# Kernel optimization log

Measured on AMD Instinct MI355X. Metric: run time of the kernel, lower is better.

Reference implementation:

```python
import jax, jax.numpy as jnp
import numpy as np

B, S, H, NH, HD, ROT = 4, 1024, 2048, 16, 128, 64
P = NH * HD  # attention projection size = 2048
EPS = 1e-6


def setup_inputs() -> dict:
    key = jax.random.key(0)
    ks = jax.random.split(key, 12)
    T = B * S
    # rotary frequency table [max_pos=S, 1, ROT]
    inv_freq = 1.0 / (10000.0 ** (np.arange(0, ROT, 2, dtype=np.float32) / ROT))
    f = np.outer(np.arange(S, dtype=np.float32), inv_freq)  # [S, ROT/2]
    freqs = np.concatenate([f, f], axis=-1)[:, None, :].astype(np.float32)
    sc = 0.02
    return {
        "positions": jnp.tile(jnp.arange(S, dtype=jnp.int64), B),  # per-seq positions 0..S-1
        "hidden_states": jax.random.normal(ks[0], (T, H), jnp.float32),
        "rotary_pos_emb": jnp.asarray(freqs),
        "lf1_cache": jax.random.normal(ks[1], (B, 1, H), jnp.float32) * sc,
        "lf2_cache": jax.random.normal(ks[2], (B, 1, H // 2), jnp.float32) * sc,
        "Wqk": jax.random.normal(ks[3], (2 * P, H), jnp.float32) * sc,
        "Wv": jax.random.normal(ks[4], (P, H), jnp.float32) * sc,
        "Wo": jax.random.normal(ks[5], (H, P), jnp.float32) * sc,
        "conv1_w": jax.random.normal(ks[6], (H // 2, H, 2), jnp.float32) * sc,  # [out, in, tap]
        "conv1_b": jnp.zeros((H // 2,), jnp.float32),
        "conv2_w": jax.random.normal(ks[7], (H, H // 2, 2), jnp.float32) * sc,
        "conv2_b": jnp.zeros((H,), jnp.float32),
        "ln_g": jnp.ones((H,), jnp.float32),
    }


def reference(positions, hidden_states, rotary_pos_emb, lf1_cache, lf2_cache,
              Wqk, Wv, Wo, conv1_w, conv1_b, conv2_w, conv2_b, ln_g):
    T = hidden_states.shape[0]
    scaling = HD ** -0.5

    # v projection on raw hidden states (done before lf_gate in the source)
    v = hidden_states @ Wv.T  # [T, P]

    # ---- LocalizedFiltering (two causal 2-tap convs + residual + RMSNorm),
    # vectorized over all sequences (source loops per sequence) ----
    x = hidden_states.reshape(B, S, H)
    xc = jnp.concatenate([lf1_cache, x], axis=1)  # [B, S+1, H]
    o1 = (jnp.einsum('bsh,oh->bso', xc[:, :-1], conv1_w[..., 0])
          + jnp.einsum('bsh,oh->bso', xc[:, 1:], conv1_w[..., 1]) + conv1_b)  # [B,S,H/2]
    o1c = jnp.concatenate([lf2_cache, o1], axis=1)  # [B, S+1, H/2]
    o2 = (jnp.einsum('bsc,oc->bso', o1c[:, :-1], conv2_w[..., 0])
          + jnp.einsum('bsc,oc->bso', o1c[:, 1:], conv2_w[..., 1]) + conv2_b)  # [B,S,H]
    o3 = o2 + x
    lf = o3 * jax.lax.rsqrt(jnp.mean(o3 * o3, axis=-1, keepdims=True) + EPS) * ln_g

    hs = lf.reshape(T, H)
    qk = (hs @ Wqk.T).reshape(T, NH, 2 * HD)
    q, k = jnp.split(qk, 2, axis=-1)  # each [T, NH, HD]

    # partial rotary (mscale = 1.0 since use_yarn=False)
    f = rotary_pos_emb[positions]            # [T, 1, ROT]
    cos, sin = jnp.cos(f), jnp.sin(f)

    def rope(t):
        tr, tp = t[..., :ROT], t[..., ROT:]
        t1, t2 = jnp.split(tr, 2, axis=-1)
        rot = jnp.concatenate([-t2, t1], axis=-1)
        return jnp.concatenate([tr * cos + rot * sin, tp], axis=-1)

    qb = rope(q).reshape(B, S, NH, HD)
    kb = rope(k).reshape(B, S, NH, HD)
    vb = v.reshape(B, S, NH, HD)

    # causal attention per sequence
    scores = jnp.einsum('bqhd,bkhd->bhqk', qb, kb) * scaling
    mask = jnp.tril(jnp.ones((S, S), bool))
    scores = jnp.where(mask, scores, jnp.finfo(scores.dtype).min)
    attn = jax.nn.softmax(scores, axis=-1)
    out = jnp.einsum('bhqk,bkhd->bqhd', attn, vb).reshape(T, P)
    return out @ Wo.T  # [T, H]
```

## Files before the change

### kernel.cpp

```cpp
#include <hip/hip_runtime.h>

typedef __bf16 bf16;
typedef __bf16 bf16x8 __attribute__((ext_vector_type(8)));
typedef __bf16 bf16x4 __attribute__((ext_vector_type(4)));
typedef float f32x4 __attribute__((ext_vector_type(4)));

#define DEVI __device__ __forceinline__

constexpr int Bc = 4, Sc = 1024, Hc = 2048, NHc = 16, HDc = 128;
constexpr int Tc = Bc * Sc;
constexpr int Pc = NHc * HDc;

DEVI void async16(const void* g, void* l) {
  __builtin_amdgcn_global_load_lds(
      (const __attribute__((address_space(1))) unsigned int*)g,
      (__attribute__((address_space(3))) unsigned int*)l, 16, 0, 0);
}

template <int WM, int WN, int MREP, int NREP, bool OUT_BF16>
__global__ __launch_bounds__(WM * WN * 64, 2) void gemm_pipe(
    const bf16* __restrict__ A, const bf16* __restrict__ W, void* __restrict__ Cout,
    const float* __restrict__ bias, int M, int N, int K) {
  constexpr int BM = WM * MREP * 16;
  constexpr int BN = WN * NREP * 16;
  constexpr int THREADS = WM * WN * 64;
  constexpr int ROWS = BM + BN;
  constexpr int CHA = BM * 4 / THREADS;
  constexpr int CHB = BN * 4 / THREADS;
  static_assert(CHA + CHB == 4, "vmcnt ledger assumes 4 loads/thread/stage");
  __shared__ bf16 lds[4][ROWS * 32];

  const int nbx = N / BN;
  const int nwg = (M / BM) * nbx;
  const int wgid = (blockIdx.x & 7) * (nwg >> 3) + (blockIdx.x >> 3);
  const int bx = wgid % nbx, by = wgid / nbx;
  const int m0 = by * BM, n0 = bx * BN;
  const int tid = threadIdx.x;
  const int w = tid >> 6, l = tid & 63;
  const int wm = w / WN, wn = w % WN;
  const int lr = l & 15;
  const int hi = l >> 4;

  auto stage = [&](int slot, int t) {
    const int k0 = t << 5;
#pragma unroll
    for (int c = 0; c < CHA; ++c) {
      const int ch = c * THREADS + tid;
      const int row = ch >> 2, cg = ch & 3;
      const int gc = (cg ^ ((row >> 1) & 3)) << 3;
      async16(A + (size_t)(m0 + row) * K + k0 + gc, (char*)&lds[slot][0] + ch * 16);
    }
#pragma unroll
    for (int c = 0; c < CHB; ++c) {
      const int ch = c * THREADS + tid;
      const int row = ch >> 2, cg = ch & 3;
      const int gc = (cg ^ ((row >> 1) & 3)) << 3;
      async16(W + (size_t)(n0 + row) * K + k0 + gc,
              (char*)&lds[slot][0] + (BM * 4 + ch) * 16);
    }
  };

  f32x4 acc[MREP][NREP] = {};
  const int nk = K >> 5;

  stage(0, 0);
  stage(1, 1);
  stage(2, 2);
  asm volatile("s_waitcnt vmcnt(8)" ::: "memory");
  __builtin_amdgcn_s_barrier();
  __builtin_amdgcn_sched_barrier(0);

  bf16x8 fAc[MREP], fBc[NREP], fAn[MREP], fBn[NREP];
  {
    const char* nb = (const char*)&lds[0][0];
#pragma unroll
    for (int mi = 0; mi < MREP; ++mi) {
      const int r = wm * (MREP * 16) + mi * 16 + lr;
      fAc[mi] = *(const bf16x8*)(nb + r * 64 + ((hi ^ ((r >> 1) & 3)) << 4));
    }
#pragma unroll
    for (int ni = 0; ni < NREP; ++ni) {
      const int r = BM + wn * (NREP * 16) + ni * 16 + lr;
      fBc[ni] = *(const bf16x8*)(nb + r * 64 + ((hi ^ ((r >> 1) & 3)) << 4));
    }
  }

#define GSTEP(T_, CA, CB, NA, NB)                                              \
  do {                                                                         \
    if ((T_) + 2 < nk) asm volatile("s_waitcnt vmcnt(4)" ::: "memory");        \
    else               asm volatile("s_waitcnt vmcnt(0)" ::: "memory");        \
    __builtin_amdgcn_s_barrier();                                              \
    __builtin_amdgcn_sched_barrier(0);                                         \
    if ((T_) + 3 < nk) stage(((T_) + 3) & 3, (T_) + 3);                        \
    if ((T_) + 1 < nk) {                                                       \
      const char* nb = (const char*)&lds[((T_) + 1) & 3][0];                   \
      _Pragma("unroll") for (int mi = 0; mi < MREP; ++mi) {                    \
        const int r = wm * (MREP * 16) + mi * 16 + lr;                         \
        NA[mi] = *(const bf16x8*)(nb + r * 64 + ((hi ^ ((r >> 1) & 3)) << 4)); \
      }                                                                        \
      _Pragma("unroll") for (int ni = 0; ni < NREP; ++ni) {                    \
        const int r = BM + wn * (NREP * 16) + ni * 16 + lr;                    \
        NB[ni] = *(const bf16x8*)(nb + r * 64 + ((hi ^ ((r >> 1) & 3)) << 4)); \
      }                                                                        \
    }                                                                          \
    __builtin_amdgcn_s_setprio(1);                                             \
    _Pragma("unroll") for (int mi = 0; mi < MREP; ++mi)                        \
      _Pragma("unroll") for (int ni = 0; ni < NREP; ++ni)                      \
        acc[mi][ni] =                                                          \
            __builtin_amdgcn_mfma_f32_16x16x32_bf16(CA[mi], CB[ni], acc[mi][ni], 0, 0, 0); \
    __builtin_amdgcn_s_setprio(0);                                             \
  } while (0)

  for (int t = 0; t < nk; t += 2) {
    GSTEP(t, fAc, fBc, fAn, fBn);
    GSTEP(t + 1, fAn, fBn, fAc, fBc);
  }
#undef GSTEP

#pragma unroll
  for (int ni = 0; ni < NREP; ++ni) {
    const int col = n0 + wn * (NREP * 16) + ni * 16 + lr;
    const float bv = bias ? bias[col] : 0.f;
#pragma unroll
    for (int mi = 0; mi < MREP; ++mi) {
#pragma unroll
      for (int j = 0; j < 4; ++j) {
        const int row = m0 + wm * (MREP * 16) + mi * 16 + (hi << 2) + j;
        const float vv = acc[mi][ni][j] + bv;
        if (OUT_BF16)
          ((bf16*)Cout)[(size_t)row * N + col] = (bf16)vv;
        else
          ((float*)Cout)[(size_t)row * N + col] = vv;
      }
    }
  }
}

__global__ void k_f2b4(const float* __restrict__ in, bf16* __restrict__ out, int n4) {
  int i = blockIdx.x * 256 + threadIdx.x;
  if (i >= n4) return;
  float4 v = ((const float4*)in)[i];
  bf16x4 o = {(bf16)v.x, (bf16)v.y, (bf16)v.z, (bf16)v.w};
  ((bf16x4*)out)[i] = o;
}

__global__ void k_build_a1(const float* __restrict__ hid, const float* __restrict__ lf1,
                           bf16* __restrict__ hsb, bf16* __restrict__ A1) {
  int idx = blockIdx.x * 256 + threadIdx.x;
  int t = idx >> 11, h = idx & 2047;
  float x = hid[idx];
  hsb[idx] = (bf16)x;
  float xp;
  if ((t & (Sc - 1)) == 0)
    xp = lf1[(t >> 10) * Hc + h];
  else
    xp = hid[idx - Hc];
  size_t a = ((size_t)t << 12) + 2 * h;
  A1[a] = (bf16)xp;
  A1[a + 1] = (bf16)x;
}

__global__ void k_build_a2(const bf16* __restrict__ o1, const float* __restrict__ lf2,
                           bf16* __restrict__ A2) {
  int idx = blockIdx.x * 256 + threadIdx.x;
  int t = idx >> 10, c = idx & 1023;
  bf16 cur = o1[idx];
  bf16 prev;
  if ((t & (Sc - 1)) == 0)
    prev = (bf16)lf2[(t >> 10) * 1024 + c];
  else
    prev = o1[idx - 1024];
  size_t a = ((size_t)t << 11) + 2 * c;
  A2[a] = prev;
  A2[a + 1] = cur;
}

__global__ __launch_bounds__(256) void k_rmsnorm(const bf16* __restrict__ o2,
                                                 const float* __restrict__ hid,
                                                 const float* __restrict__ g,
                                                 bf16* __restrict__ lf) {
  int t = blockIdx.x, tid = threadIdx.x;
  size_t base = ((size_t)t << 11) + tid * 8;
  bf16x8 ov = *(const bf16x8*)&o2[base];
  const float* hp = &hid[base];
  float vals[8];
  float ss = 0.f;
#pragma unroll
  for (int i = 0; i < 8; ++i) {
    float x = (float)ov[i] + hp[i];
    vals[i] = x;
    ss += x * x;
  }
#pragma unroll
  for (int off = 1; off < 64; off <<= 1) ss += __shfl_xor(ss, off);
  __shared__ float red[4];
  if ((tid & 63) == 0) red[tid >> 6] = ss;
  __syncthreads();
  float tot = red[0] + red[1] + red[2] + red[3];
  float inv = rsqrtf(tot * (1.f / 2048.f) + 1e-6f);
  bf16x8 o;
#pragma unroll
  for (int i = 0; i < 8; ++i) o[i] = (bf16)(vals[i] * inv * g[tid * 8 + i]);
  *(bf16x8*)&lf[base] = o;
}

__global__ void k_rope(const bf16* __restrict__ qk, const float* __restrict__ rot,
                       bf16* __restrict__ qr, bf16* __restrict__ kr) {
  int bid = blockIdx.x;
  int n = bid & 15, t = bid >> 4;
  int s = t & (Sc - 1), b = t >> 10;
  int tid = threadIdx.x;
  int isk = tid >> 7, d = tid & 127;
  const bf16* src = qk + ((size_t)t << 12) + n * 256 + isk * 128;
  float val = (float)src[d];
  float outv = val;
  if (d < 64) {
    float f = rot[s * 64 + d];
    float c = cosf(f), sn = sinf(f);
    float other = (float)src[d ^ 32];
    outv = (d < 32) ? (val * c - other * sn) : (val * c + other * sn);
  }
  bf16* dst = isk ? kr : qr;
  dst[((size_t)((b * 16 + n) * 1024 + s) << 7) + d] = (bf16)outv;
}

__global__ void k_vt(const bf16* __restrict__ v, bf16* __restrict__ vT) {
  __shared__ bf16 tile[32][33];
  int bid = blockIdx.x;
  int dt = bid & 3;
  int st = (bid >> 2) & 31;
  int bn = bid >> 7;
  int b = bn >> 4, n = bn & 15;
  int tx = threadIdx.x & 31, ty = threadIdx.x >> 5;
#pragma unroll
  for (int i = 0; i < 4; ++i) {
    int s = st * 32 + ty + i * 8;
    int d = dt * 32 + tx;
    tile[ty + i * 8][tx] = v[(size_t)(b * 1024 + s) * 2048 + n * 128 + d];
  }
  __syncthreads();
#pragma unroll
  for (int i = 0; i < 4; ++i) {
    int d = dt * 32 + ty + i * 8;
    int s = st * 32 + tx;
    vT[((size_t)(bn * 128 + d)) * 1024 + s] = tile[tx][ty + i * 8];
  }
}

__global__ __launch_bounds__(256, 2) void k_attn(const bf16* __restrict__ qr,
                                                 const bf16* __restrict__ kr,
                                                 const bf16* __restrict__ vT,
                                                 bf16* __restrict__ att) {
  __shared__ bf16 Ks[2][64 * 128];
  __shared__ bf16 Vs[2][128 * 64];
  __shared__ bf16 plds[4][16 * 64];
  const int bid = blockIdx.x;
  const int xcd = bid & 7, jj = bid >> 3;
  const int bn = xcd * 8 + (jj >> 3);
  const int pr = jj & 7;
  const int tid = threadIdx.x, w = tid >> 6, l = tid & 63;
  const int lr = l & 15, hi = l >> 4;
  const bf16* kb = kr + ((size_t)bn << 17);
  const bf16* vb = vT + ((size_t)bn << 17);
  const int b = bn >> 4, hh = bn & 15;
  const float scaling = 0.08838834764831845f;

  auto stage = [&](int buf, int kt) {
#pragma unroll
    for (int c = 0; c < 4; ++c) {
      int chunk = c * 256 + tid;
      int prow = chunk >> 4, pcg = chunk & 15;
      async16(kb + ((size_t)(kt * 64 + prow) << 7) + ((pcg ^ (prow & 7)) << 3),
              (char*)&Ks[buf][0] + chunk * 16);
    }
#pragma unroll
    for (int c = 0; c < 4; ++c) {
      int chunk = c * 256 + tid;
      int prow = chunk >> 3, pcg = chunk & 7;
      async16(vb + ((size_t)prow << 10) + kt * 64 + ((pcg ^ (prow & 7)) << 3),
              (char*)&Vs[buf][0] + chunk * 16);
    }
  };

#pragma unroll 1
  for (int phase = 0; phase < 2; ++phase) {
    const int qt = phase ? (15 - pr) : pr;
    const int qg0 = qt * 64 + w * 16;
    const bf16* qb = qr + ((size_t)(bn * 1024 + qg0) << 7);
    bf16x8 qf[4];
#pragma unroll
    for (int ks = 0; ks < 4; ++ks) qf[ks] = *(const bf16x8*)&qb[lr * 128 + ks * 32 + hi * 8];
    f32x4 oacc[8] = {};
    float mrow[4] = {-1e30f, -1e30f, -1e30f, -1e30f};
    float lrow[4] = {0.f, 0.f, 0.f, 0.f};
    const int nkb = qt + 1;

    stage(0, 0);
    __syncthreads();

    for (int kbt = 0; kbt < nkb; ++kbt) {
      const int cur = kbt & 1;
      if (kbt + 1 < nkb) stage(cur ^ 1, kbt + 1);

      f32x4 sacc[4] = {};
#pragma unroll
      for (int n = 0; n < 4; ++n) {
        const int krow = n * 16 + lr;
#pragma unroll
        for (int ks = 0; ks < 4; ++ks) {
          bf16x8 kf = *(const bf16x8*)&Ks[cur][(krow << 7) + ((((ks << 2) | hi) ^ (krow & 7)) << 3)];
          sacc[n] = __builtin_amdgcn_mfma_f32_16x16x32_bf16(qf[ks], kf, sacc[n], 0, 0, 0);
        }
      }
      const bool needmask = (kbt * 64 + 63 > qg0);
#pragma unroll
      for (int n = 0; n < 4; ++n) {
        int kg = kbt * 64 + n * 16 + lr;
#pragma unroll
        for (int j = 0; j < 4; ++j) {
          float sv = sacc[n][j] * scaling;
          if (needmask && kg > qg0 + hi * 4 + j) sv = -1e30f;
          sacc[n][j] = sv;
        }
      }
      float sf[4];
#pragma unroll
      for (int j = 0; j < 4; ++j) {
        float pm = fmaxf(fmaxf(sacc[0][j], sacc[1][j]), fmaxf(sacc[2][j], sacc[3][j]));
        pm = fmaxf(pm, __shfl_xor(pm, 1));
        pm = fmaxf(pm, __shfl_xor(pm, 2));
        pm = fmaxf(pm, __shfl_xor(pm, 4));
        pm = fmaxf(pm, __shfl_xor(pm, 8));
        float mn = fmaxf(mrow[j], pm);
        sf[j] = __expf(mrow[j] - mn);
        mrow[j] = mn;
      }
#pragma unroll
      for (int n = 0; n < 4; ++n)
#pragma unroll
        for (int j = 0; j < 4; ++j) sacc[n][j] = __expf(sacc[n][j] - mrow[j]);
#pragma unroll
      for (int j = 0; j < 4; ++j) {
        float ps = sacc[0][j] + sacc[1][j] + sacc[2][j] + sacc[3][j];
        ps += __shfl_xor(ps, 1);
        ps += __shfl_xor(ps, 2);
        ps += __shfl_xor(ps, 4);
        ps += __shfl_xor(ps, 8);
        lrow[j] = lrow[j] * sf[j] + ps;
      }
#pragma unroll
      for (int dt = 0; dt < 8; ++dt)
#pragma unroll
        for (int j = 0; j < 4; ++j) oacc[dt][j] *= sf[j];
#pragma unroll
      for (int n = 0; n < 4; ++n)
#pragma unroll
        for (int j = 0; j < 4; ++j)
          plds[w][(hi * 4 + j) * 64 + n * 16 + lr] = (bf16)sacc[n][j];
      asm volatile("s_waitcnt lgkmcnt(0)" ::: "memory");
#pragma unroll
      for (int ks2 = 0; ks2 < 2; ++ks2) {
        bf16x8 pf = *(const bf16x8*)&plds[w][lr * 64 + ks2 * 32 + hi * 8];
#pragma unroll
        for (int dt = 0; dt < 8; ++dt) {
          const int vrow = dt * 16 + lr;
          bf16x8 vf = *(const bf16x8*)&Vs[cur][(vrow << 6) + ((((ks2 << 2) | hi) ^ (lr & 7)) << 3)];
          oacc[dt] = __builtin_amdgcn_mfma_f32_16x16x32_bf16(pf, vf, oacc[dt], 0, 0, 0);
        }
      }
      __syncthreads();
    }

#pragma unroll
    for (int j = 0; j < 4; ++j) {
      float inv = 1.f / lrow[j];
      int qg = qg0 + hi * 4 + j;
      size_t obase = ((size_t)(b * 1024 + qg) << 11) + hh * 128;
#pragma unroll
      for (int dt = 0; dt < 8; ++dt) att[obase + dt * 16 + lr] = (bf16)(oacc[dt][j] * inv);
    }
  }
}

extern "C" void kernel_launch(void* const* d_in, const int* in_sizes, int n_in,
                              void* d_out, int out_size, void* d_ws, size_t ws_size,
                              hipStream_t stream) {
  const float* hid = (const float*)d_in[1];
  const float* rot = (const float*)d_in[2];
  const float* lf1 = (const float*)d_in[3];
  const float* lf2 = (const float*)d_in[4];
  const float* Wqk = (const float*)d_in[5];
  const float* Wv  = (const float*)d_in[6];
  const float* Wo  = (const float*)d_in[7];
  const float* c1w = (const float*)d_in[8];
  const float* c1b = (const float*)d_in[9];
  const float* c2w = (const float*)d_in[10];
  const float* c2b = (const float*)d_in[11];
  const float* lng = (const float*)d_in[12];
  float* outp = (float*)d_out;
  char* ws = (char*)d_ws;

  const size_t MB = 1ull << 20;
  bf16* Wslot = (bf16*)(ws + 0 * MB);
  bf16* A1    = (bf16*)(ws + 16 * MB);
  bf16* qkb   = A1;
  bf16* hsb   = (bf16*)(ws + 48 * MB);
  bf16* lfb   = hsb;
  bf16* vT    = hsb;
  bf16* v     = (bf16*)(ws + 64 * MB);
  bf16* att   = v;
  bf16* o1    = (bf16*)(ws + 80 * MB);
  bf16* A2    = (bf16*)(ws + 88 * MB);
  bf16* qr    = A2;
  bf16* o2    = (bf16*)(ws + 104 * MB);
  bf16* kr    = o2;

  auto f2b = [&](const float* in, bf16* out, int n) {
    int n4 = n / 4;
    k_f2b4<<<(n4 + 255) / 256, 256, 0, stream>>>(in, out, n4);
  };

  f2b(Wv, Wslot, 2048 * 2048);
  k_build_a1<<<Tc * Hc / 256, 256, 0, stream>>>(hid, lf1, hsb, A1);
  gemm_pipe<2, 2, 4, 4, true><<<512, 256, 0, stream>>>(hsb, Wslot, v, nullptr, Tc, Pc, Hc);

  f2b(c1w, Wslot, 1024 * 2048 * 2);
  gemm_pipe<2, 2, 4, 4, true><<<256, 256, 0, stream>>>(A1, Wslot, o1, c1b, Tc, 1024, 4096);

  k_build_a2<<<Tc * 1024 / 256, 256, 0, stream>>>(o1, lf2, A2);
  f2b(c2w, Wslot, 2048 * 1024 * 2);
  gemm_pipe<2, 2, 4, 4, true><<<512, 256, 0, stream>>>(A2, Wslot, o2, c2b, Tc, 2048, 2048);

  k_rmsnorm<<<Tc, 256, 0, stream>>>(o2, hid, lng, lfb);

  f2b(Wqk, Wslot, 4096 * 2048);
  gemm_pipe<2, 4, 8, 4, true><<<256, 512, 0, stream>>>(lfb, Wslot, qkb, nullptr, Tc, 4096, Hc);

  k_rope<<<Tc * NHc, 256, 0, stream>>>(qkb, rot, qr, kr);
  k_vt<<<64 * 32 * 4, 256, 0, stream>>>(v, vT);
  k_attn<<<Bc * NHc * 8, 256, 0, stream>>>(qr, kr, vT, att);

  f2b(Wo, Wslot, 2048 * 2048);
  gemm_pipe<2, 2, 4, 4, false><<<512, 256, 0, stream>>>(att, Wslot, outp, nullptr, Tc, 2048, 2048);
}
```

Before: 401.9 us.

## Add 8-wave double-buffered GEMM with quadrant-interleaved loads and MFMA

Introduces a new GEMM kernel using 512 threads (8 waves), 256x128 or 256x256 tiles, a 64-wide K step with XOR-swizzled LDS and double buffering. Each K step is split into four quadrant phases that interleave LDS fragment loads, half-tile prefetch of the next stage, and MFMA bursts raised to higher priority. The v, conv2, qk and output projections switch to it with larger tiles and fewer workgroups. The goal is better latency hiding and more data reuse per tile. In exchange the kernel needs more barriers, and a fixed 256-workgroup grid may limit occupancy.

```diff
diff --git a/kernel.cpp b/kernel.cpp
--- a/kernel.cpp
+++ b/kernel.cpp
@@ -15,6 +15,155 @@
   __builtin_amdgcn_global_load_lds(
       (const __attribute__((address_space(1))) unsigned int*)g,
       (__attribute__((address_space(3))) unsigned int*)l, 16, 0, 0);
+}
+
+#define BAR() __builtin_amdgcn_s_barrier()
+#define LGKM0()                                          \
+  do {                                                   \
+    asm volatile("s_waitcnt lgkmcnt(0)" ::: "memory");   \
+    __builtin_amdgcn_sched_barrier(0);                   \
+  } while (0)
+#define VM0() asm volatile("s_waitcnt vmcnt(0)" ::: "memory")
+
+template <int WM, int WN, int MREP, int NREP, bool OUT_BF16>
+__global__ __launch_bounds__(512, 2) void gemm8(
+    const bf16* __restrict__ A, const bf16* __restrict__ W, void* __restrict__ Cout,
+    const float* __restrict__ bias, int M, int N, int K) {
+  constexpr int BM = WM * MREP * 16;
+  constexpr int BN = WN * NREP * 16;
+  constexpr int MH = MREP / 2, NH = NREP / 2;
+  constexpr int LA = BM / 128;
+  constexpr int LB = BN / 128;
+  __shared__ char lds[2][(BM + BN) * 128];
+
+  const int nbx = N / BN;
+  const int nwg = (M / BM) * nbx;
+  const int wgid = (blockIdx.x & 7) * (nwg >> 3) + (blockIdx.x >> 3);
+  const int bx = wgid % nbx, by = wgid / nbx;
+  const int m0 = by * BM, n0 = bx * BN;
+  const int tid = threadIdx.x;
+  const int w = tid >> 6, l = tid & 63;
+  const int wm = w / WN, wn = w % WN;
+  const int lr = l & 15, hi = l >> 4;
+
+  auto stageA = [&](int buf, int t, int half) {
+#pragma unroll
+    for (int c = 0; c < LA; ++c) {
+      const int ch = c * 512 + tid;
+      const int row = half * (BM / 2) + (ch >> 3);
+      const int grp = ch & 7;
+      async16(A + (size_t)(m0 + row) * K + (t << 6) + ((grp ^ (row & 7)) << 3),
+              &lds[buf][row * 128 + grp * 16]);
+    }
+  };
+  auto stageB = [&](int buf, int t, int half) {
+#pragma unroll
+    for (int c = 0; c < LB; ++c) {
+      const int ch = c * 512 + tid;
+      const int row = half * (BN / 2) + (ch >> 3);
+      const int grp = ch & 7;
+      async16(W + (size_t)(n0 + row) * K + (t << 6) + ((grp ^ (row & 7)) << 3),
+              &lds[buf][BM * 128 + row * 128 + grp * 16]);
+    }
+  };
+  auto LD = [&](const char* Lp, int row, int g) -> bf16x8 {
+    return *(const bf16x8*)(Lp + ((size_t)row << 7) + ((g ^ (row & 7)) << 4));
+  };
+
+#define QUAD(MB_, NB_, FB_)                                                     \
+  do {                                                                          \
+    __builtin_amdgcn_s_setprio(1);                                              \
+    _Pragma("unroll") for (int m = 0; m < MH; ++m)                              \
+      _Pragma("unroll") for (int n = 0; n < NH; ++n)                            \
+        _Pragma("unroll") for (int kk = 0; kk < 2; ++kk)                        \
+          acc[(MB_) + m][(NB_) + n] = __builtin_amdgcn_mfma_f32_16x16x32_bf16(  \
+              fa[m][kk], FB_[n][kk], acc[(MB_) + m][(NB_) + n], 0, 0, 0);       \
+    __builtin_amdgcn_s_setprio(0);                                              \
+  } while (0)
+
+  f32x4 acc[MREP][NREP] = {};
+  bf16x8 fa[MH][2], fb0[NH][2], fb1[NH][2];
+  const int nk = K >> 6;
+
+  stageA(0, 0, 0);
+  stageB(0, 0, 0);
+  stageB(0, 0, 1);
+  stageA(0, 0, 1);
+  VM0();
+  BAR();
+
+#pragma unroll 1
+  for (int t = 0; t < nk; ++t) {
+    const char* Lb = lds[t & 1];
+    const int nbuf = (t & 1) ^ 1;
+    const bool pf = (t + 1 < nk);
+#pragma unroll
+    for (int m = 0; m < MH; ++m) {
+      const int r = wm * (MREP * 16) + m * 16 + lr;
+      fa[m][0] = LD(Lb, r, hi);
+      fa[m][1] = LD(Lb, r, 4 + hi);
+    }
+#pragma unroll
+    for (int n = 0; n < NH; ++n) {
+      const int r = BM + wn * (NREP * 16) + n * 16 + lr;
+      fb0[n][0] = LD(Lb, r, hi);
+      fb0[n][1] = LD(Lb, r, 4 + hi);
+    }
+    if (pf) {
+      stageA(nbuf, t + 1, 0);
+      stageB(nbuf, t + 1, 0);
+    }
+    BAR();
+    LGKM0();
+    QUAD(0, 0, fb0);
+    BAR();
+#pragma unroll
+    for (int n = 0; n < NH; ++n) {
+      const int r = BM + wn * (NREP * 16) + (NH + n) * 16 + lr;
+      fb1[n][0] = LD(Lb, r, hi);
+      fb1[n][1] = LD(Lb, r, 4 + hi);
+    }
+    if (pf) {
+      stageB(nbuf, t + 1, 1);
+      stageA(nbuf, t + 1, 1);
+    }
+    BAR();
+    LGKM0();
+    QUAD(0, NH, fb1);
+    BAR();
+#pragma unroll
+    for (int m = 0; m < MH; ++m) {
+      const int r = wm * (MREP * 16) + (MH + m) * 16 + lr;
+      fa[m][0] = LD(Lb, r, hi);
+      fa[m][1] = LD(Lb, r, 4 + hi);
+    }
+    BAR();
+    LGKM0();
+    QUAD(MH, NH, fb1);
+    BAR();
+    QUAD(MH, 0, fb0);
+    VM0();
+    BAR();
+  }
+#undef QUAD
+
+#pragma unroll
+  for (int ni = 0; ni < NREP; ++ni) {
+    const int col = n0 + wn * (NREP * 16) + ni * 16 + lr;
+    const float bv = bias ? bias[col] : 0.f;
+#pragma unroll
+    for (int mi = 0; mi < MREP; ++mi) {
+#pragma unroll
+      for (int j = 0; j < 4; ++j) {
+        const int row = m0 + wm * (MREP * 16) + mi * 16 + (hi << 2) + j;
+        const float vv = acc[mi][ni][j] + bv;
+        if (OUT_BF16)
+          ((bf16*)Cout)[(size_t)row * N + col] = (bf16)vv;
+        else
+          ((float*)Cout)[(size_t)row * N + col] = vv;
+      }
+    }
+  }
 }
 
 template <int WM, int WN, int MREP, int NREP, bool OUT_BF16>
@@ -422,24 +571,24 @@
 
   f2b(Wv, Wslot, 2048 * 2048);
   k_build_a1<<<Tc * Hc / 256, 256, 0, stream>>>(hid, lf1, hsb, A1);
-  gemm_pipe<2, 2, 4, 4, true><<<512, 256, 0, stream>>>(hsb, Wslot, v, nullptr, Tc, Pc, Hc);
+  gemm8<4, 2, 4, 4, true><<<256, 512, 0, stream>>>(hsb, Wslot, v, nullptr, Tc, Pc, Hc);
 
   f2b(c1w, Wslot, 1024 * 2048 * 2);
   gemm_pipe<2, 2, 4, 4, true><<<256, 256, 0, stream>>>(A1, Wslot, o1, c1b, Tc, 1024, 4096);
 
   k_build_a2<<<Tc * 1024 / 256, 256, 0, stream>>>(o1, lf2, A2);
   f2b(c2w, Wslot, 2048 * 1024 * 2);
-  gemm_pipe<2, 2, 4, 4, true><<<512, 256, 0, stream>>>(A2, Wslot, o2, c2b, Tc, 2048, 2048);
+  gemm8<4, 2, 4, 4, true><<<256, 512, 0, stream>>>(A2, Wslot, o2, c2b, Tc, 2048, 2048);
 
   k_rmsnorm<<<Tc, 256, 0, stream>>>(o2, hid, lng, lfb);
 
   f2b(Wqk, Wslot, 4096 * 2048);
-  gemm_pipe<2, 4, 8, 4, true><<<256, 512, 0, stream>>>(lfb, Wslot, qkb, nullptr, Tc, 4096, Hc);
+  gemm8<2, 4, 8, 4, true><<<256, 512, 0, stream>>>(lfb, Wslot, qkb, nullptr, Tc, 4096, Hc);
 
   k_rope<<<Tc * NHc, 256, 0, stream>>>(qkb, rot, qr, kr);
   k_vt<<<64 * 32 * 4, 256, 0, stream>>>(v, vT);
   k_attn<<<Bc * NHc * 8, 256, 0, stream>>>(qr, kr, vT, att);
 
   f2b(Wo, Wslot, 2048 * 2048);
-  gemm_pipe<2, 2, 4, 4, false><<<512, 256, 0, stream>>>(att, Wslot, outp, nullptr, Tc, 2048, 2048);
-}
+  gemm8<4, 2, 4, 4, false><<<256, 512, 0, stream>>>(att, Wslot, outp, nullptr, Tc, 2048, 2048);
+}
```

Measured after the change: 391.3 us. -2.6%, faster.
